# Kernel optimization log

Measured on AMD Instinct MI355X. Metric: run time of the kernel, lower is better.

The kernel has to match this reference:

```python
import jax, jax.numpy as jnp
import numpy as np

B, S, HID = 1, 2048, 1024
HQ, HKV, D = 16, 8, 64
W = 64          # causal window size (includes self at offset 0)
K = 128         # total neighbors per query: W window + (K-W) random rewires


def setup_inputs() -> dict:
    key = jax.random.key(0)
    ks = jax.random.split(key, 8)
    hidden_states = jax.random.normal(ks[0], (B, S, HID), jnp.float32)
    sc = HID ** -0.5
    q_w = jax.random.normal(ks[1], (HQ * D, HID), jnp.float32) * sc
    k_w = jax.random.normal(ks[2], (HKV * D, HID), jnp.float32) * sc
    v_w = jax.random.normal(ks[3], (HKV * D, HID), jnp.float32) * sc
    o_w = jax.random.normal(ks[4], (HQ * D, HID), jnp.float32).T * sc  # [HID, HQ*D] -> stored as [HID, HQ*D]? keep [HID, HQ*D]
    o_w = jax.random.normal(ks[4], (HID, HQ * D), jnp.float32) * sc
    edge_bias = jax.random.normal(ks[5], (4,), jnp.float32) * 0.1
    # neighbor indices: per kv-head, per query position.
    pos = jnp.arange(S)
    win = pos[:, None] - jnp.arange(W)[None, :]                    # [S, W], offset 0 == self
    win = jnp.broadcast_to(win[None], (HKV, S, W))
    rew = jax.random.randint(ks[6], (HKV, S, K - W), 0, S)         # random rewire edges
    neigh_idx = jnp.concatenate([win, rew], axis=-1).astype(jnp.int32)  # [HKV, S, K]
    edge_type = jnp.concatenate([
        jnp.full((HKV, S, W), 1, jnp.int32),       # 'window'
        jnp.full((HKV, S, K - W), 3, jnp.int32),   # 'rewire'
    ], axis=-1)
    return {
        'hidden_states': hidden_states, 'q_w': q_w, 'k_w': k_w, 'v_w': v_w,
        'o_w': o_w, 'edge_bias': edge_bias, 'neigh_idx': neigh_idx,
        'edge_type': edge_type,
    }


def reference(hidden_states, q_w, k_w, v_w, o_w, edge_bias, neigh_idx, edge_type):
    b, s, _ = hidden_states.shape
    hkv, _, kk = neigh_idx.shape
    hq = q_w.shape[0] // (k_w.shape[0] // hkv)
    d = k_w.shape[0] // hkv
    hq = q_w.shape[0] // d
    g = hq // hkv
    scaling = d ** -0.5

    # projections (nn.Linear: x @ W.T)
    q = (hidden_states @ q_w.T).reshape(b, s, hq, d).transpose(0, 2, 1, 3)    # [B,HQ,S,D]
    k = (hidden_states @ k_w.T).reshape(b, s, hkv, d).transpose(0, 2, 1, 3)   # [B,HKV,S,D]
    v = (hidden_states @ v_w.T).reshape(b, s, hkv, d).transpose(0, 2, 1, 3)

    # causal neighbor mask + safe clamp (mirrors _causal_neighbor_mask / _safe_neighbor_idx)
    pos = jnp.arange(s)
    mask = (neigh_idx >= 0) & (neigh_idx < s) & (neigh_idx <= pos[None, :, None])  # [HKV,S,K]
    safe = jnp.clip(neigh_idx, 0, s - 1)

    # gather K/V at neighbor indices: [B,HKV,S,K,D]
    h_idx = jnp.arange(hkv)[:, None, None]
    k_g = k[:, h_idx, safe, :]
    v_g = v[:, h_idx, safe, :]

    # GQA: group query heads over kv heads
    qg = q.reshape(b, hkv, g, s, d)
    scores = jnp.einsum('bhgsd,bhskd->bhgsk', qg, k_g) * scaling              # [B,HKV,G,S,K]
    scores = scores + edge_bias[edge_type][None, :, None, :, :]
    neg = jnp.finfo(scores.dtype).min
    scores = jnp.where(mask[None, :, None, :, :], scores, neg)
    attn = jax.nn.softmax(scores, axis=-1)

    out = jnp.einsum('bhgsk,bhskd->bhgsd', attn, v_g)                         # [B,HKV,G,S,D]
    out = out.reshape(b, hq, s, d).transpose(0, 2, 1, 3).reshape(b, s, hq * d)
    return out @ o_w.T                                                        # [B,S,HID]
```

## Files before the change

### kernel.cpp

```cpp
#include <hip/hip_runtime.h>
#include <hip/hip_bf16.h>

#define S_LEN 2048
#define HIDDEN 1024

typedef __attribute__((ext_vector_type(4))) float f32x4;
typedef __attribute__((ext_vector_type(8))) _Float16 f16x8;
typedef __attribute__((ext_vector_type(2))) _Float16 f16x2;
typedef __attribute__((ext_vector_type(2))) __fp16 fp16x2;
typedef unsigned short u16;
typedef unsigned int u32;

typedef const __attribute__((address_space(1))) unsigned int as1_u32;
typedef __attribute__((address_space(3))) unsigned int as3_u32;

__device__ __forceinline__ u16 f2h(float f) {
  union { _Float16 h; u16 u; } c; c.h = (_Float16)f; return c.u;
}
__device__ __forceinline__ f16x2 u2h2(u32 u) {
  union { u32 x; f16x2 h; } c; c.x = u; return c.h;
}
__device__ __forceinline__ float fdot2(u32 a, u32 b, float c) {
#if __has_builtin(__builtin_amdgcn_fdot2)
  return __builtin_amdgcn_fdot2(u2h2(a), u2h2(b), c, false);
#else
  f16x2 ha = u2h2(a), hb = u2h2(b);
  return fmaf((float)ha.x, (float)hb.x, fmaf((float)ha.y, (float)hb.y, c));
#endif
}
__device__ __forceinline__ u32 pkrtz(float a, float b) {
#if __has_builtin(__builtin_amdgcn_cvt_pkrtz)
  union { fp16x2 h; u32 u; } c;
  c.h = __builtin_amdgcn_cvt_pkrtz(a, b);
  return c.u;
#else
  union { f16x2 h; u32 u; } c;
  c.h.x = (_Float16)a; c.h.y = (_Float16)b;
  return c.u;
#endif
}

__global__ __launch_bounds__(256) void cvt_all(
    const float* __restrict__ h, const float* __restrict__ qw,
    const float* __restrict__ kw, const float* __restrict__ vw,
    const float* __restrict__ ow, u16* __restrict__ hb, u16* __restrict__ qwb,
    u16* __restrict__ kwb, u16* __restrict__ vwb, u16* __restrict__ owb) {
  const int b = blockIdx.x;
  const float* src; u16* dst; int base;
  if (b < 2048)      { src = h;  dst = hb;  base = b; }
  else if (b < 3072) { src = qw; dst = qwb; base = b - 2048; }
  else if (b < 3584) { src = kw; dst = kwb; base = b - 3072; }
  else if (b < 4096) { src = vw; dst = vwb; base = b - 3584; }
  else               { src = ow; dst = owb; base = b - 4096; }
  const int i = base * 256 + threadIdx.x;
  const float4 v = ((const float4*)src)[i];
  ushort4 r;
  r.x = f2h(v.x); r.y = f2h(v.y); r.z = f2h(v.z); r.w = f2h(v.w);
  ((ushort4*)dst)[i] = r;
}

template <int BM, bool OUT_F16>
__device__ __forceinline__ void gemm_core(
    u16* __restrict__ As, u16* __restrict__ Bs,
    const u16* __restrict__ A, const u16* __restrict__ W, void* __restrict__ Cv,
    int Kd, int ldc, int mtile, int ntile) {
  constexpr int MF = BM / 32;
  const int tid = threadIdx.x;
  const int lane = tid & 63;
  const int wave = tid >> 6;
  const int wr = wave >> 1, wc = wave & 1;
  f32x4 acc[MF][4] = {};
  const int m0 = mtile * BM, n0 = ntile * 128;
  const int nk = Kd >> 5;

  auto stage = [&](int buf, int kt) {
    u16* Ad = As + buf * (BM * 32);
    u16* Bd = Bs + buf * (128 * 32);
#pragma unroll
    for (int i = 0; i < BM / 64; ++i) {
      const int e = (i * 256 + tid) * 8;
      const int r = e >> 5, c = e & 31;
      __builtin_amdgcn_global_load_lds(
          (as1_u32*)(A + (size_t)(m0 + r) * Kd + kt * 32 + c), (as3_u32*)(Ad + e), 16, 0, 0);
    }
#pragma unroll
    for (int i = 0; i < 2; ++i) {
      const int e = (i * 256 + tid) * 8;
      const int r = e >> 5, c = e & 31;
      __builtin_amdgcn_global_load_lds(
          (as1_u32*)(W + (size_t)(n0 + r) * Kd + kt * 32 + c), (as3_u32*)(Bd + e), 16, 0, 0);
    }
  };

  stage(0, 0);
  __syncthreads();
  int cur = 0;
  for (int kt = 0; kt < nk; ++kt) {
    if (kt + 1 < nk) stage(cur ^ 1, kt + 1);
    const u16* Ac = As + cur * (BM * 32);
    const u16* Bc = Bs + cur * (128 * 32);
    f16x8 af[MF], bfr[4];
#pragma unroll
    for (int mi = 0; mi < MF; ++mi)
      af[mi] = *(const f16x8*)(Ac + (wr * (BM / 2) + mi * 16 + (lane & 15)) * 32 + (lane >> 4) * 8);
#pragma unroll
    for (int ni = 0; ni < 4; ++ni)
      bfr[ni] = *(const f16x8*)(Bc + (wc * 64 + ni * 16 + (lane & 15)) * 32 + (lane >> 4) * 8);
#pragma unroll
    for (int mi = 0; mi < MF; ++mi)
#pragma unroll
      for (int ni = 0; ni < 4; ++ni)
        acc[mi][ni] = __builtin_amdgcn_mfma_f32_16x16x32_f16(af[mi], bfr[ni], acc[mi][ni], 0, 0, 0);
    __syncthreads();
    cur ^= 1;
  }

#pragma unroll
  for (int mi = 0; mi < MF; ++mi) {
#pragma unroll
    for (int ni = 0; ni < 4; ++ni) {
      const int row0 = m0 + wr * (BM / 2) + mi * 16 + (lane >> 4) * 4;
      const int col = n0 + wc * 64 + ni * 16 + (lane & 15);
#pragma unroll
      for (int r = 0; r < 4; ++r) {
        if (OUT_F16)
          ((u16*)Cv)[(size_t)(row0 + r) * ldc + col] = f2h(acc[mi][ni][r]);
        else
          ((float*)Cv)[(size_t)(row0 + r) * ldc + col] = acc[mi][ni][r];
      }
    }
  }
}

__global__ __launch_bounds__(256, 2) void qkv_gemm(
    const u16* __restrict__ hb, const u16* __restrict__ qwb,
    const u16* __restrict__ kwb, const u16* __restrict__ vwb,
    u16* __restrict__ Qb, u16* __restrict__ Kb, u16* __restrict__ Vb) {
  __shared__ u16 As[2 * 128 * 32];
  __shared__ u16 Bs[2 * 128 * 32];
  const int nt = blockIdx.x, mt = blockIdx.y;
  if (nt < 8)       gemm_core<128, true>(As, Bs, hb, qwb, Qb, HIDDEN, 1024, mt, nt);
  else if (nt < 12) gemm_core<128, true>(As, Bs, hb, kwb, Kb, HIDDEN, 512, mt, nt - 8);
  else              gemm_core<128, true>(As, Bs, hb, vwb, Vb, HIDDEN, 512, mt, nt - 12);
}

__global__ __launch_bounds__(256, 2) void o_gemm(
    const u16* __restrict__ attnb, const u16* __restrict__ owb,
    float* __restrict__ out) {
  __shared__ u16 As[2 * 64 * 32];
  __shared__ u16 Bs[2 * 128 * 32];
  gemm_core<64, false>(As, Bs, attnb, owb, out, HIDDEN, 1024, blockIdx.y, blockIdx.x);
}

__global__ __launch_bounds__(256) void attn_kernel(
    const u16* __restrict__ Qb, const u16* __restrict__ Kb,
    const u16* __restrict__ Vb, const int* __restrict__ neigh,
    const float* __restrict__ ebias, u16* __restrict__ attnb) {
  __shared__ u32 park[4][192];

  const int tid = threadIdx.x;
  const int lane = tid & 63;
  const int wv = tid >> 6;
  const int h = blockIdx.y;
  const int su = __builtin_amdgcn_readfirstlane(blockIdx.x * 4 + wv);

  const u16* Kp = Kb + h * 64;
  const u16* Vp = Vb + h * 64;

  const int iB = neigh[((size_t)h * S_LEN + su) * 128 + 64 + lane];
  const bool okB = (iB >= 0) && (iB <= su);
  const int gB = min(max(iB, 0), S_LEN - 1);
  const bool okA = lane <= su;
  const int gA = max(su - lane, 0);

  const u16* qp = Qb + (size_t)su * 1024 + h * 128;
  const u16* kwp = Kp + (size_t)gA * 512;
  const u16* krp = Kp + (size_t)gB * 512;
  float sA0 = 0.f, sA1 = 0.f, sB0 = 0.f, sB1 = 0.f;
#pragma unroll
  for (int t = 0; t < 8; ++t) {
    const uint4 kw = *(const uint4*)(kwp + t * 8);
    const uint4 kr = *(const uint4*)(krp + t * 8);
    const uint4 qa = *(const uint4*)(qp + t * 8);
    const uint4 qb = *(const uint4*)(qp + 64 + t * 8);
    sA0 = fdot2(kw.x, qa.x, sA0); sA0 = fdot2(kw.y, qa.y, sA0);
    sA0 = fdot2(kw.z, qa.z, sA0); sA0 = fdot2(kw.w, qa.w, sA0);
    sA1 = fdot2(kw.x, qb.x, sA1); sA1 = fdot2(kw.y, qb.y, sA1);
    sA1 = fdot2(kw.z, qb.z, sA1); sA1 = fdot2(kw.w, qb.w, sA1);
    sB0 = fdot2(kr.x, qa.x, sB0); sB0 = fdot2(kr.y, qa.y, sB0);
    sB0 = fdot2(kr.z, qa.z, sB0); sB0 = fdot2(kr.w, qa.w, sB0);
    sB1 = fdot2(kr.x, qb.x, sB1); sB1 = fdot2(kr.y, qb.y, sB1);
    sB1 = fdot2(kr.z, qb.z, sB1); sB1 = fdot2(kr.w, qb.w, sB1);
  }

  const float NEG = -1e30f;
  const float SC = 0.125f;
  const float ebW = ebias[1];
  const float ebR = ebias[3];
  sA0 = okA ? fmaf(sA0, SC, ebW) : NEG;
  sA1 = okA ? fmaf(sA1, SC, ebW) : NEG;
  sB0 = okB ? fmaf(sB0, SC, ebR) : NEG;
  sB1 = okB ? fmaf(sB1, SC, ebR) : NEG;

  float m0 = fmaxf(sA0, sB0), m1 = fmaxf(sA1, sB1);
#pragma unroll
  for (int off = 32; off; off >>= 1) {
    m0 = fmaxf(m0, __shfl_xor(m0, off));
    m1 = fmaxf(m1, __shfl_xor(m1, off));
  }
  float eA0 = __expf(sA0 - m0), eB0 = __expf(sB0 - m0);
  float eA1 = __expf(sA1 - m1), eB1 = __expf(sB1 - m1);
  float d0 = eA0 + eB0, d1 = eA1 + eB1;
#pragma unroll
  for (int off = 32; off; off >>= 1) {
    d0 += __shfl_xor(d0, off);
    d1 += __shfl_xor(d1, off);
  }
  const float rc0 = 1.0f / d0, rc1 = 1.0f / d1;

  u32* pb = park[wv];
  int* ib = (int*)(park[wv] + 128);
  const float pA0 = eA0 * rc0, pA1 = eA1 * rc1;
  const float pB0 = eB0 * rc0, pB1 = eB1 * rc1;
  const float hA0 = __shfl_xor(pA0, 1), hA1 = __shfl_xor(pA1, 1);
  const float hB0 = __shfl_xor(pB0, 1), hB1 = __shfl_xor(pB1, 1);
  ib[lane] = gB;
  if (!(lane & 1)) {
    uint4 pk;
    pk.x = pkrtz(pA0, hA0);
    pk.y = pkrtz(pA1, hA1);
    pk.z = pkrtz(pB0, hB0);
    pk.w = pkrtz(pB1, hB1);
    *(uint4*)(pb + (lane >> 1) * 4) = pk;
  }
  asm volatile("s_waitcnt lgkmcnt(0)" ::: "memory");

  float a0 = 0.f, a1 = 0.f;
#pragma unroll 4
  for (int m = 0; m < 32; ++m) {
    const uint4 pp = *(const uint4*)(pb + m * 4);
    const int2 rB = *(const int2*)(ib + m * 2);
    const int r0w = max(su - 2 * m, 0);
    const int r1w = max(su - 2 * m - 1, 0);
    const u32 w0 = Vp[(size_t)r0w * 512 + lane];
    const u32 w1 = Vp[(size_t)r1w * 512 + lane];
    const u32 b0 = Vp[(size_t)rB.x * 512 + lane];
    const u32 b1 = Vp[(size_t)rB.y * 512 + lane];
    const u32 wpair = (w1 << 16) | w0;
    const u32 bpair = (b1 << 16) | b0;
    a0 = fdot2(wpair, pp.x, a0);
    a1 = fdot2(wpair, pp.y, a1);
    a0 = fdot2(bpair, pp.z, a0);
    a1 = fdot2(bpair, pp.w, a1);
  }

  u16* op = attnb + (size_t)su * 1024 + h * 128;
  op[lane] = f2h(a0);
  op[64 + lane] = f2h(a1);
}

extern "C" void kernel_launch(void* const* d_in, const int* in_sizes, int n_in,
                              void* d_out, int out_size, void* d_ws, size_t ws_size,
                              hipStream_t stream) {
  const float* hidden = (const float*)d_in[0];
  const float* q_w = (const float*)d_in[1];
  const float* k_w = (const float*)d_in[2];
  const float* v_w = (const float*)d_in[3];
  const float* o_w = (const float*)d_in[4];
  const float* ebias = (const float*)d_in[5];
  const int* neigh = (const int*)d_in[6];
  float* out = (float*)d_out;

  char* ws = (char*)d_ws;
  u16* hb    = (u16*)(ws + (0ull << 20));
  u16* qwb   = (u16*)(ws + (4ull << 20));
  u16* kwb   = (u16*)(ws + (6ull << 20));
  u16* vwb   = (u16*)(ws + (7ull << 20));
  u16* owb   = (u16*)(ws + (8ull << 20));
  u16* Qb    = (u16*)(ws + (10ull << 20));
  u16* Kb    = (u16*)(ws + (14ull << 20));
  u16* Vb    = (u16*)(ws + (16ull << 20));
  u16* attnb = (u16*)(ws + (18ull << 20));

  cvt_all<<<5120, 256, 0, stream>>>(hidden, q_w, k_w, v_w, o_w,
                                    hb, qwb, kwb, vwb, owb);
  qkv_gemm<<<dim3(16, 16), 256, 0, stream>>>(hb, qwb, kwb, vwb, Qb, Kb, Vb);
  attn_kernel<<<dim3(512, 8), 256, 0, stream>>>(Qb, Kb, Vb, neigh, ebias, attnb);
  o_gemm<<<dim3(8, 32), 256, 0, stream>>>(attnb, owb, out);
}
```

Baseline: 106.1 us.

## Stage window and rewire K rows into swizzled LDS via async global-to-LDS loads

```diff
diff --git a/kernel.cpp b/kernel.cpp
--- a/kernel.cpp
+++ b/kernel.cpp
@@ -152,17 +152,21 @@
   gemm_core<64, false>(As, Bs, attnb, owb, out, HIDDEN, 1024, blockIdx.y, blockIdx.x);
 }
 
+#define WIN_ROWS 72
+#define WIN_ELEMS (WIN_ROWS * 64)
 __global__ __launch_bounds__(256) void attn_kernel(
     const u16* __restrict__ Qb, const u16* __restrict__ Kb,
     const u16* __restrict__ Vb, const int* __restrict__ neigh,
     const float* __restrict__ ebias, u16* __restrict__ attnb) {
-  __shared__ u32 park[4][192];
+  __shared__ u16 kwin[WIN_ELEMS];
+  __shared__ u16 krand[4][4096];
 
   const int tid = threadIdx.x;
   const int lane = tid & 63;
   const int wv = tid >> 6;
   const int h = blockIdx.y;
-  const int su = __builtin_amdgcn_readfirstlane(blockIdx.x * 4 + wv);
+  const int s0 = blockIdx.x * 4;
+  const int su = __builtin_amdgcn_readfirstlane(s0 + wv);
 
   const u16* Kp = Kb + h * 64;
   const u16* Vp = Vb + h * 64;
@@ -171,16 +175,48 @@
   const bool okB = (iB >= 0) && (iB <= su);
   const int gB = min(max(iB, 0), S_LEN - 1);
   const bool okA = lane <= su;
-  const int gA = max(su - lane, 0);
+
+  u16* krw = krand[wv];
+  const int chunk = (lane & 7) ^ (lane >> 3);
+
+#pragma unroll
+  for (int gg = 0; gg < 2; ++gg) {
+    const int g = wv + gg * 4;
+    const int r_lds = g * 8 + (lane >> 3);
+    const int row = min(max(s0 - 63 + r_lds, 0), S_LEN - 1);
+    __builtin_amdgcn_global_load_lds(
+        (as1_u32*)(Kp + (size_t)row * 512 + chunk * 8),
+        (as3_u32*)(kwin + g * 512 + lane * 8), 16, 0, 0);
+  }
+  if (wv == 0) {
+    const int g = 8;
+    const int r_lds = g * 8 + (lane >> 3);
+    const int row = min(max(s0 - 63 + r_lds, 0), S_LEN - 1);
+    __builtin_amdgcn_global_load_lds(
+        (as1_u32*)(Kp + (size_t)row * 512 + chunk * 8),
+        (as3_u32*)(kwin + g * 512 + lane * 8), 16, 0, 0);
+  }
+
+#pragma unroll
+  for (int g2 = 0; g2 < 8; ++g2) {
+    const int row = __shfl(gB, g2 * 8 + (lane >> 3));
+    __builtin_amdgcn_global_load_lds(
+        (as1_u32*)(Kp + (size_t)row * 512 + chunk * 8),
+        (as3_u32*)(krw + g2 * 512 + lane * 8), 16, 0, 0);
+  }
+
+  __syncthreads();
 
   const u16* qp = Qb + (size_t)su * 1024 + h * 128;
-  const u16* kwp = Kp + (size_t)gA * 512;
-  const u16* krp = Kp + (size_t)gB * 512;
+  const int rW = wv + 63 - lane;
+  const u16* kwrow = kwin + rW * 64;
+  const u16* krrow = krw + lane * 64;
+  const int rw7 = rW & 7, ln7 = lane & 7;
   float sA0 = 0.f, sA1 = 0.f, sB0 = 0.f, sB1 = 0.f;
 #pragma unroll
   for (int t = 0; t < 8; ++t) {
-    const uint4 kw = *(const uint4*)(kwp + t * 8);
-    const uint4 kr = *(const uint4*)(krp + t * 8);
+    const uint4 kw = *(const uint4*)(kwrow + ((t ^ rw7) << 3));
+    const uint4 kr = *(const uint4*)(krrow + ((t ^ ln7) << 3));
     const uint4 qa = *(const uint4*)(qp + t * 8);
     const uint4 qb = *(const uint4*)(qp + 64 + t * 8);
     sA0 = fdot2(kw.x, qa.x, sA0); sA0 = fdot2(kw.y, qa.y, sA0);
@@ -218,8 +254,9 @@
   }
   const float rc0 = 1.0f / d0, rc1 = 1.0f / d1;
 
-  u32* pb = park[wv];
-  int* ib = (int*)(park[wv] + 128);
+  asm volatile("s_waitcnt lgkmcnt(0)" ::: "memory");
+  u32* pb = (u32*)krw;
+  int* ib = (int*)(krw + 512);
   const float pA0 = eA0 * rc0, pA1 = eA1 * rc1;
   const float pB0 = eB0 * rc0, pB1 = eB1 * rc1;
   const float hA0 = __shfl_xor(pA0, 1), hA1 = __shfl_xor(pA1, 1);
@@ -239,13 +276,14 @@
 #pragma unroll 4
   for (int m = 0; m < 32; ++m) {
     const uint4 pp = *(const uint4*)(pb + m * 4);
-    const int2 rB = *(const int2*)(ib + m * 2);
+    const int rbx = __builtin_amdgcn_readfirstlane(ib[m * 2]);
+    const int rby = __builtin_amdgcn_readfirstlane(ib[m * 2 + 1]);
     const int r0w = max(su - 2 * m, 0);
     const int r1w = max(su - 2 * m - 1, 0);
     const u32 w0 = Vp[(size_t)r0w * 512 + lane];
     const u32 w1 = Vp[(size_t)r1w * 512 + lane];
-    const u32 b0 = Vp[(size_t)rB.x * 512 + lane];
-    const u32 b1 = Vp[(size_t)rB.y * 512 + lane];
+    const u32 b0 = Vp[(size_t)rbx * 512 + lane];
+    const u32 b1 = Vp[(size_t)rby * 512 + lane];
     const u32 wpair = (w1 << 16) | w0;
     const u32 bpair = (b1 << 16) | b0;
     a0 = fdot2(wpair, pp.x, a0);
```

Result: faster. 95.55 us (-9.9%).
